# Kernel tuning notes

Measured on AMD Instinct MI355X. Metric: run time of the kernel, lower is better.

## Reference

```python
import jax, jax.numpy as jnp
import numpy as np


def ste_sign(x):
    # Forward: sign(x); backward: identity (straight-through estimator).
    return jax.lax.stop_gradient(jnp.sign(x) - x) + x


def setup_inputs() -> dict:
    key = jax.random.key(0)
    k1, k2 = jax.random.split(key)
    x = jax.random.normal(k1, (8192, 4096), dtype=jnp.float32)
    weight = jax.random.normal(k2, (4096, 4096), dtype=jnp.float32) * 0.02
    return {"x": x, "weight": weight}


def reference(x, weight):
    # binary_linear: sign(x) @ sign(weight).T  (F.linear semantics)
    x_bin = ste_sign(x)          # [N, in]
    w_bin = ste_sign(weight)     # [out, in]
    return jnp.einsum('ni,oi->no', x_bin, w_bin)
```

## Files before the change

kernel.cpp:

```cpp
#include <hip/hip_runtime.h>
#include <hip/hip_bf16.h>
#include <stdint.h>

typedef int i32x4 __attribute__((ext_vector_type(4)));
typedef int i32x8 __attribute__((ext_vector_type(8)));
typedef float f32x4 __attribute__((ext_vector_type(4)));

__device__ __forceinline__ unsigned int sign_nib(float x) {
  return x > 0.0f ? 0x2u : (x < 0.0f ? 0xAu : 0x0u);
}

__device__ __forceinline__ unsigned int pack8(const float4& a, const float4& b) {
  return sign_nib(a.x)
       | (sign_nib(a.y) << 4)
       | (sign_nib(a.z) << 8)
       | (sign_nib(a.w) << 12)
       | (sign_nib(b.x) << 16)
       | (sign_nib(b.y) << 20)
       | (sign_nib(b.z) << 24)
       | (sign_nib(b.w) << 28);
}

__global__ __launch_bounds__(256)
void binarize_fp4(const float* __restrict__ in,
                  uint2* __restrict__ out,
                  int ngroups) {
  int idx = blockIdx.x * blockDim.x + threadIdx.x;
  int stride = gridDim.x * blockDim.x;
  const float4* in4 = (const float4*)in;
  for (int g = idx; g < ngroups; g += stride) {
    float4 v0 = in4[4 * g];
    float4 v1 = in4[4 * g + 1];
    float4 v2 = in4[4 * g + 2];
    float4 v3 = in4[4 * g + 3];
    uint2 o;
    o.x = pack8(v0, v1);
    o.y = pack8(v2, v3);
    out[g] = o;
  }
}

__device__ __forceinline__ void load_lds16(const void* g, void* l) {
  __builtin_amdgcn_global_load_lds(
      (const __attribute__((address_space(1))) void*)g,
      (__attribute__((address_space(3))) void*)l,
      16, 0, 0);
}

__device__ __forceinline__ void bar() {
  asm volatile("s_barrier" ::: "memory");
}
template <int N>
__device__ __forceinline__ void waitvm() {
  asm volatile("s_waitcnt vmcnt(%0)" ::"i"(N) : "memory");
}

__device__ __forceinline__ i32x8 rd8(const char* p) {
  i32x4 q = *(const i32x4*)p;
  return __builtin_shufflevector(q, q, 0, 1, 2, 3, -1, -1, -1, -1);
}

__global__ __launch_bounds__(512, 2)
void gemm_bt_fp4(const unsigned char* __restrict__ A,
                 const unsigned char* __restrict__ B,
                 float* __restrict__ C,
                 int M, int N, int K, int nbn) {
  constexpr int BM = 256, BN = 256;
  __shared__ __attribute__((aligned(16))) char lds[4 * 32768];

  int nwg = gridDim.x;
  int bid = blockIdx.x;
  int cpx = nwg >> 3;
  int swz = (bid & 7) * cpx + (bid >> 3);
  int tm = swz / nbn;
  int tn = swz % nbn;

  const int t = threadIdx.x;
  const int lane = t & 63;
  const int wid = t >> 6;
  const int wm = wid >> 2;
  const int wn = wid & 3;
  const int lrow = lane & 15;
  const int kg = lane >> 4;

  const int Kb = K >> 1;
  const size_t rowA0 = (size_t)tm * BM;
  const size_t rowB0 = (size_t)tn * BN;

  f32x4 acc[8][4] = {};

  const int nt = K / 128;

  const int soff0 = wid * 1024 + lane * 16;
  const int srow0 = soff0 >> 6;
  const int scb0 = ((soff0 >> 4) & 3) ^ ((srow0 >> 1) & 3);
  const int soff1 = 8192 + wid * 1024 + lane * 16;
  const int srow1 = soff1 >> 6;
  const int scb1 = ((soff1 >> 4) & 3) ^ ((srow1 >> 1) & 3);

  auto stage = [&](int tt) {
    const int b = tt & 3;
    const int k0b = tt * 64;
    load_lds16(A + (rowA0 + srow0) * Kb + k0b + scb0 * 16,
               lds + b * 32768 + wid * 1024);
    load_lds16(A + (rowA0 + srow1) * Kb + k0b + scb1 * 16,
               lds + b * 32768 + 8192 + wid * 1024);
    load_lds16(B + (rowB0 + srow0) * Kb + k0b + scb0 * 16,
               lds + b * 32768 + 16384 + wid * 1024);
    load_lds16(B + (rowB0 + srow1) * Kb + k0b + scb1 * 16,
               lds + b * 32768 + 16384 + 8192 + wid * 1024);
  };

  const int rcol = ((kg ^ ((lrow >> 1) & 3)) << 4);
  const int aoff = (wm * 128 + lrow) * 64 + rcol;
  const int boff = 16384 + (wn * 64 + lrow) * 64 + rcol;

  const int SC = 0x7F7F7F7F;

  stage(0); stage(1);

  for (int tt = 0; tt < nt; ++tt) {
    const int b = tt & 3;
    if (tt + 1 < nt) waitvm<4>(); else waitvm<0>();
    bar();

    const char* Ab = lds + b * 32768 + aoff;
    const char* Bb = lds + b * 32768 + boff;

    i32x8 bf[4], af[4];
    #pragma unroll
    for (int n = 0; n < 4; ++n)
      bf[n] = rd8(Bb + n * 1024);
    #pragma unroll
    for (int m = 0; m < 4; ++m)
      af[m] = rd8(Ab + m * 1024);

    if (tt + 2 < nt) stage(tt + 2);

    #pragma unroll
    for (int m = 0; m < 4; ++m)
      #pragma unroll
      for (int n = 0; n < 4; ++n)
        acc[m][n] = __builtin_amdgcn_mfma_scale_f32_16x16x128_f8f6f4(
            af[m], bf[n], acc[m][n], 4, 4, 0, SC, 0, SC);

    i32x8 ag[4];
    #pragma unroll
    for (int m = 0; m < 4; ++m)
      ag[m] = rd8(Ab + (m + 4) * 1024);

    #pragma unroll
    for (int m = 0; m < 4; ++m)
      #pragma unroll
      for (int n = 0; n < 4; ++n)
        acc[m + 4][n] = __builtin_amdgcn_mfma_scale_f32_16x16x128_f8f6f4(
            ag[m], bf[n], acc[m + 4][n], 4, 4, 0, SC, 0, SC);
  }

  const size_t cRow0 = rowA0 + (size_t)wm * 128;
  const size_t cCol0 = rowB0 + (size_t)wn * 64;
  const int orow = kg * 4;
  #pragma unroll
  for (int m = 0; m < 8; ++m)
    #pragma unroll
    for (int n = 0; n < 4; ++n)
      #pragma unroll
      for (int r = 0; r < 4; ++r)
        C[(cRow0 + m * 16 + orow + r) * N + cCol0 + n * 16 + lrow] =
            acc[m][n][r];
}

extern "C" void kernel_launch(void* const* d_in, const int* in_sizes, int n_in,
                              void* d_out, int out_size, void* d_ws, size_t ws_size,
                              hipStream_t stream) {
  const float* x = (const float*)d_in[0];
  const float* w = (const float*)d_in[1];
  float* out = (float*)d_out;

  const int K = 4096;
  const int M = in_sizes[0] / K;
  const int N = in_sizes[1] / K;

  unsigned char* xb = (unsigned char*)d_ws;
  unsigned char* wb = xb + (size_t)M * (K / 2);

  int gx = (M * K) / 16;
  int gw = (N * K) / 16;
  binarize_fp4<<<dim3(2048), dim3(256), 0, stream>>>(x, (uint2*)xb, gx);
  binarize_fp4<<<dim3(2048), dim3(256), 0, stream>>>(w, (uint2*)wb, gw);

  int nbm = M / 256;
  int nbn = N / 256;
  gemm_bt_fp4<<<dim3(nbm * nbn), dim3(512), 0, stream>>>(
      xb, wb, out, M, N, K, nbn);
}
```

Baseline: 123.2 us.

## Split binarization into int8 sign pass plus int8-to-fp4 repack kernel

Replaces the direct float-to-fp4 packing kernel with two stages. The first writes int8 signs to an intermediate buffer, and the second repacks those int8 values into fp4 nibbles with bit tricks in one launch covering both x and weight. This adds an extra kernel launch and an extra round trip of int8 data through memory. It may have been meant to simplify the per-element packing, but it increases total memory traffic.

```diff
diff --git a/kernel.cpp b/kernel.cpp
--- a/kernel.cpp
+++ b/kernel.cpp
@@ -6,37 +6,50 @@
 typedef int i32x8 __attribute__((ext_vector_type(8)));
 typedef float f32x4 __attribute__((ext_vector_type(4)));
 
-__device__ __forceinline__ unsigned int sign_nib(float x) {
-  return x > 0.0f ? 0x2u : (x < 0.0f ? 0xAu : 0x0u);
-}
-
-__device__ __forceinline__ unsigned int pack8(const float4& a, const float4& b) {
-  return sign_nib(a.x)
-       | (sign_nib(a.y) << 4)
-       | (sign_nib(a.z) << 8)
-       | (sign_nib(a.w) << 12)
-       | (sign_nib(b.x) << 16)
-       | (sign_nib(b.y) << 20)
-       | (sign_nib(b.z) << 24)
-       | (sign_nib(b.w) << 28);
-}
-
-__global__ __launch_bounds__(256)
-void binarize_fp4(const float* __restrict__ in,
-                  uint2* __restrict__ out,
-                  int ngroups) {
+__device__ __forceinline__ signed char sign_i8(float x) {
+  return x > 0.0f ? (signed char)1 : (x < 0.0f ? (signed char)-1 : (signed char)0);
+}
+
+__global__ void binarize_i8(const float* __restrict__ in,
+                            signed char* __restrict__ out,
+                            int n8) {
   int idx = blockIdx.x * blockDim.x + threadIdx.x;
   int stride = gridDim.x * blockDim.x;
   const float4* in4 = (const float4*)in;
-  for (int g = idx; g < ngroups; g += stride) {
-    float4 v0 = in4[4 * g];
-    float4 v1 = in4[4 * g + 1];
-    float4 v2 = in4[4 * g + 2];
-    float4 v3 = in4[4 * g + 3];
+  uint2* out2 = (uint2*)out;
+  for (int i = idx; i < n8; i += stride) {
+    float4 a = in4[2 * i];
+    float4 b = in4[2 * i + 1];
+    union { signed char c[8]; uint2 u; } p;
+    p.c[0] = sign_i8(a.x); p.c[1] = sign_i8(a.y);
+    p.c[2] = sign_i8(a.z); p.c[3] = sign_i8(a.w);
+    p.c[4] = sign_i8(b.x); p.c[5] = sign_i8(b.y);
+    p.c[6] = sign_i8(b.z); p.c[7] = sign_i8(b.w);
+    out2[i] = p.u;
+  }
+}
+
+__device__ __forceinline__ unsigned int nib4(unsigned int u) {
+  unsigned int nz = (((u & 0x7f7f7f7fu) + 0x7f7f7f7fu) | u) & 0x80808080u;
+  return (nz >> 6) | ((u & 0x80808080u) >> 4);
+}
+__device__ __forceinline__ unsigned int p16(unsigned int u) {
+  unsigned int n = nib4(u);
+  unsigned int r = (n | (n >> 4)) & 0x00FF00FFu;
+  return (r | (r >> 8)) & 0xFFFFu;
+}
+
+__global__ void repack_i8_fp4(const uint4* __restrict__ in,
+                              uint2* __restrict__ out,
+                              int n16) {
+  int idx = blockIdx.x * blockDim.x + threadIdx.x;
+  int stride = gridDim.x * blockDim.x;
+  for (int i = idx; i < n16; i += stride) {
+    uint4 v = in[i];
     uint2 o;
-    o.x = pack8(v0, v1);
-    o.y = pack8(v2, v3);
-    out[g] = o;
+    o.x = p16(v.x) | (p16(v.y) << 16);
+    o.y = p16(v.z) | (p16(v.w) << 16);
+    out[i] = o;
   }
 }
 
@@ -181,16 +194,22 @@
   const int M = in_sizes[0] / K;
   const int N = in_sizes[1] / K;
 
-  unsigned char* xb = (unsigned char*)d_ws;
-  unsigned char* wb = xb + (size_t)M * (K / 2);
-
-  int gx = (M * K) / 16;
-  int gw = (N * K) / 16;
-  binarize_fp4<<<dim3(2048), dim3(256), 0, stream>>>(x, (uint2*)xb, gx);
-  binarize_fp4<<<dim3(2048), dim3(256), 0, stream>>>(w, (uint2*)wb, gw);
+  unsigned char* xb4 = (unsigned char*)d_ws;
+  unsigned char* wb4 = xb4 + (size_t)M * (K / 2);
+  signed char* xb8 = (signed char*)(wb4 + (size_t)N * (K / 2));
+  signed char* wb8 = xb8 + (size_t)M * K;
+
+  int n8x = (M * K) / 8;
+  int n8w = (N * K) / 8;
+  binarize_i8<<<dim3(2048), dim3(256), 0, stream>>>(x, xb8, n8x);
+  binarize_i8<<<dim3(2048), dim3(256), 0, stream>>>(w, wb8, n8w);
+
+  int n16 = (M * K + N * K) / 16;
+  repack_i8_fp4<<<dim3(2048), dim3(256), 0, stream>>>(
+      (const uint4*)xb8, (uint2*)xb4, n16);
 
   int nbm = M / 256;
   int nbn = N / 256;
   gemm_bt_fp4<<<dim3(nbm * nbn), dim3(512), 0, stream>>>(
-      xb, wb, out, M, N, K, nbn);
-}
+      xb4, wb4, out, M, N, K, nbn);
+}
```

Result: slower. 140.0 us (+13.7%).
